# Optimization experiments

Measured on AMD Instinct MI355X. Metric: run time of the kernel, lower is better.

Reference implementation:

```python
import jax, jax.numpy as jnp
import numpy as np

N = 100000
E = 1600000
B = 64
NUM_CLASSES = 10


def setup_inputs() -> dict:
    key = jax.random.key(0)
    ks = jax.random.split(key, 8)
    x = jax.random.normal(ks[0], (N, 5), dtype=jnp.float32)
    edge_index = jax.random.randint(ks[1], (2, E), 0, N, dtype=jnp.int64)
    batch = jnp.sort(jax.random.randint(ks[2], (N,), 0, B, dtype=jnp.int64))

    def glorot(k, fan_in, fan_out):
        s = jnp.sqrt(6.0 / (fan_in + fan_out)).astype(jnp.float32)
        return jax.random.uniform(k, (fan_in, fan_out), jnp.float32, -s, s)

    dims = [(5, 32), (32, 64), (64, 128), (128, 256)]
    Ws = [glorot(jax.random.fold_in(ks[3], i), a, b) for i, (a, b) in enumerate(dims)]
    bs = [jnp.zeros((b,), jnp.float32) for (_, b) in dims]
    fc1_w = glorot(ks[4], 256, 100)
    fc1_b = jnp.zeros((100,), jnp.float32)
    fc2_w = glorot(ks[5], 100, NUM_CLASSES)
    fc2_b = jnp.zeros((NUM_CLASSES,), jnp.float32)
    return {
        'x': x, 'edge_index': edge_index, 'batch': batch,
        'W1': Ws[0], 'b1': bs[0], 'W2': Ws[1], 'b2': bs[1],
        'W3': Ws[2], 'b3': bs[2], 'W4': Ws[3], 'b4': bs[3],
        'fc1_w': fc1_w, 'fc1_b': fc1_b, 'fc2_w': fc2_w, 'fc2_b': fc2_b,
    }


def _gcn_conv(x, W, b, src, dst, dinv):
    h = x @ W                                   # [N, out]
    norm = (dinv[src] * dinv[dst])[:, None]      # [E, 1]
    msg = h[src] * norm                          # gather + scale
    agg = jax.ops.segment_sum(msg, dst, num_segments=N)
    agg = agg + h * (dinv * dinv)[:, None]       # self-loop contribution
    return agg + b


def reference(x, edge_index, batch, W1, b1, W2, b2, W3, b3, W4, b4,
              fc1_w, fc1_b, fc2_w, fc2_b):
    src, dst = edge_index[0], edge_index[1]
    # degree including self-loop
    deg = jax.ops.segment_sum(jnp.ones((E,), jnp.float32), dst, num_segments=N) + 1.0
    dinv = jax.lax.rsqrt(deg)

    h = jax.nn.relu(_gcn_conv(x, W1, b1, src, dst, dinv))
    # mesh_unpool with pool target 0 -> identity
    h = jax.nn.relu(_gcn_conv(h, W2, b2, src, dst, dinv))
    h = jax.nn.relu(_gcn_conv(h, W3, b3, src, dst, dinv))
    h = jax.nn.relu(_gcn_conv(h, W4, b4, src, dst, dinv))

    # global mean pool over graphs
    sums = jax.ops.segment_sum(h, batch, num_segments=B)
    cnt = jax.ops.segment_sum(jnp.ones((N,), jnp.float32), batch, num_segments=B)
    pooled = sums / jnp.maximum(cnt, 1.0)[:, None]

    h = jax.nn.relu(pooled @ fc1_w + fc1_b)
    return jax.nn.log_softmax(h @ fc2_w + fc2_b, axis=-1)
```

## Files before the change

### kernel.cpp

```cpp
#include <hip/hip_runtime.h>
#include <hip/hip_bf16.h>
#include <cmath>

#define NN 100000
#define NE 1600000
#define NBATCH 64
#define NB 391
#define NBP 512
#define BCAP 5120
#define NPAD (NB * BCAP)

typedef __attribute__((ext_vector_type(8))) _Float16 f16x8;
typedef __attribute__((ext_vector_type(4))) float f32x4;
typedef __attribute__((ext_vector_type(2))) float f32x2;

__device__ __forceinline__ void atomAdd(float* p, float v) {
  unsafeAtomicAdd(p, v);
}

__device__ __forceinline__ unsigned char f2fp8(float f) {
  int pk = __builtin_amdgcn_cvt_pk_fp8_f32(f, f, 0, false);
  return (unsigned char)(pk & 0xff);
}

template<int W32>
__device__ __forceinline__ void ldw(const unsigned char* p, unsigned* v) {
  if constexpr (W32 == 2) {
    uint2 t = *(const uint2*)p; v[0] = t.x; v[1] = t.y;
  } else if constexpr (W32 == 4) {
    uint4 t = *(const uint4*)p; v[0] = t.x; v[1] = t.y; v[2] = t.z; v[3] = t.w;
  } else {
    uint4 t0 = *(const uint4*)p; uint4 t1 = *(const uint4*)(p + 16);
    v[0] = t0.x; v[1] = t0.y; v[2] = t0.z; v[3] = t0.w;
    v[4] = t1.x; v[5] = t1.y; v[6] = t1.z; v[7] = t1.w;
  }
}

template<int W32>
__device__ __forceinline__ void accw(const unsigned* v, f32x2* acc) {
#pragma unroll
  for (int w = 0; w < W32; ++w) {
    acc[2 * w]     += __builtin_amdgcn_cvt_pk_f32_fp8(v[w], false);
    acc[2 * w + 1] += __builtin_amdgcn_cvt_pk_f32_fp8(v[w], true);
  }
}

__global__ __launch_bounds__(256) void k_bin(const int* __restrict__ src,
    const int* __restrict__ dst, int* __restrict__ bucketCnt, unsigned* __restrict__ pairs,
    const float* __restrict__ W2, const float* __restrict__ W3, const float* __restrict__ W4,
    _Float16* __restrict__ Wt2, _Float16* __restrict__ Wt3, _Float16* __restrict__ Wt4) {
  __shared__ int hist[NBP];
  __shared__ int scn[NBP];
  __shared__ int ofs[NBP];
  __shared__ int gbase[NBP];
  __shared__ unsigned buf[4096];
  __shared__ unsigned short bufb[4096];
  const int base = blockIdx.x * 4096;
  const int n = (NE - base < 4096) ? NE - base : 4096;
  for (int i = threadIdx.x; i < NBP; i += 256) hist[i] = 0;
  __syncthreads();

  int myS[16], myD[16];
  int nloc = 0;
  for (int i = threadIdx.x, j = 0; i < n; i += 256, ++j) {
    myS[j] = src[base + i];
    myD[j] = dst[base + i];
    atomicAdd(&hist[myD[j] >> 8], 1);
    nloc = j + 1;
  }
  __syncthreads();

  scn[threadIdx.x] = hist[threadIdx.x];
  scn[threadIdx.x + 256] = hist[threadIdx.x + 256];
  __syncthreads();
  for (int off = 1; off < NBP; off <<= 1) {
    const int i0 = threadIdx.x, i1 = threadIdx.x + 256;
    int t0 = (i0 >= off) ? scn[i0 - off] : 0;
    int t1 = (i1 >= off) ? scn[i1 - off] : 0;
    __syncthreads();
    scn[i0] += t0;
    scn[i1] += t1;
    __syncthreads();
  }
  ofs[threadIdx.x] = scn[threadIdx.x] - hist[threadIdx.x];
  ofs[threadIdx.x + 256] = scn[threadIdx.x + 256] - hist[threadIdx.x + 256];
  for (int b = threadIdx.x; b < NB; b += 256) {
    int c = hist[b];
    if (c) gbase[b] = b * BCAP + atomicAdd(&bucketCnt[b], c);
  }
  __syncthreads();

  for (int j = 0; j < nloc; ++j) {
    int b = myD[j] >> 8;
    int slot = atomicAdd(&ofs[b], 1);
    buf[slot] = ((unsigned)myS[j] << 8) | ((unsigned)myD[j] & 255u);
    bufb[slot] = (unsigned short)b;
  }
  __syncthreads();

  for (int i = threadIdx.x; i < n; i += 256) {
    int b = (int)bufb[i];
    int ex = scn[b] - hist[b];
    pairs[gbase[b] + (i - ex)] = buf[i];
  }

  int idx = blockIdx.x * 256 + threadIdx.x;
  if (idx < 2048) {
    int k = idx / 64, m = idx - k * 64;
    Wt2[m * 32 + k] = (_Float16)W2[idx];
  } else if (idx < 10240) {
    int j = idx - 2048;
    int k = j / 128, m = j - k * 128;
    Wt3[m * 64 + k] = (_Float16)W3[j];
  } else if (idx < 43008) {
    int j = idx - 10240;
    int k = j / 256, m = j - k * 256;
    Wt4[m * 128 + k] = (_Float16)W4[j];
  }
}

__global__ __launch_bounds__(256) void k_cntfill(const unsigned* __restrict__ pairs,
    const int* __restrict__ bucketCnt, const int* __restrict__ batch,
    const float* __restrict__ x, int* __restrict__ rowbeg, int* __restrict__ rowend,
    float* __restrict__ dinv, int* __restrict__ csrc, float* __restrict__ pcnt,
    _Float16* __restrict__ xs8) {
  __shared__ int c[256];
  __shared__ int scn[256];
  __shared__ int rowb[256];
  __shared__ int ofs[256];
  __shared__ int h[64];
  const int tid = threadIdx.x;
  c[tid] = 0; ofs[tid] = 0;
  if (tid < 64) h[tid] = 0;
  __syncthreads();
  const int b = blockIdx.x;
  const int s = b * BCAP;
  const int e = s + bucketCnt[b];
  for (int i = s + tid; i < e; i += 256) atomicAdd(&c[pairs[i] & 255u], 1);
  __syncthreads();
  const int v = c[tid];
  scn[tid] = v;
  __syncthreads();
  for (int off = 1; off < 256; off <<= 1) {
    int t = (tid >= off) ? scn[tid - off] : 0;
    __syncthreads();
    scn[tid] += t;
    __syncthreads();
  }
  rowb[tid] = s + scn[tid] - v;
  const int node = b * 256 + tid;
  rowbeg[node] = rowb[tid];
  rowend[node] = rowb[tid] + v;
  if (node < NN) {
    const float di = rsqrtf((float)v + 1.0f);
    dinv[node] = di;
    f16x8 o = {0, 0, 0, 0, 0, 0, 0, 0};
    o[0] = (_Float16)(x[(size_t)node * 5 + 0] * di);
    o[1] = (_Float16)(x[(size_t)node * 5 + 1] * di);
    o[2] = (_Float16)(x[(size_t)node * 5 + 2] * di);
    o[3] = (_Float16)(x[(size_t)node * 5 + 3] * di);
    o[4] = (_Float16)(x[(size_t)node * 5 + 4] * di);
    *(f16x8*)(xs8 + (size_t)node * 8) = o;
    atomicAdd(&h[batch[node]], 1);
  }
  __syncthreads();
  for (int i = s + tid; i < e; i += 256) {
    unsigned p = pairs[i];
    int t = (int)(p & 255u);
    int pos = rowb[t] + atomicAdd(&ofs[t], 1);
    csrc[pos] = (int)(p >> 8);
  }
  if (tid < 64 && h[tid]) atomAdd(&pcnt[tid], (float)h[tid]);
}

struct MegaArgs {
  const _Float16* xs8;
  const int* rowbeg; const int* rowend; const int* csrc;
  const float* dinv;
  const float* W1; const float* b1;
  unsigned char* F0;
  const _Float16* Wt2; const float* b2;
  unsigned char* F1;
  const _Float16* Wt3; const float* b3;
  unsigned char* F2;
  const _Float16* Wt4; const float* b4;
  const int* batch; float* pooled; const float* pcnt;
  const float* fc1w; const float* fc1b; const float* fc2w; const float* fc2b;
  float* out;
};

__global__ __launch_bounds__(256) void kw_l1(MegaArgs a) {
  __shared__ float w_s[160];
  __shared__ float b_s[32];
  const int tid = threadIdx.x;
  if (tid < 160) w_s[tid] = a.W1[tid];
  if (tid < 32) b_s[tid] = a.b1[tid];
  __syncthreads();
  const int r = blockIdx.x * 256 + tid;
  if (r >= NN) return;
  const float di = a.dinv[r];
  f16x8 av = *(const f16x8*)(a.xs8 + (size_t)r * 8);
  f16x8 cacc = {0, 0, 0, 0, 0, 0, 0, 0};
  int e = a.rowbeg[r];
  const int e1 = a.rowend[r];
  for (; e + 2 <= e1; e += 2) {
    const int s0 = a.csrc[e], s1 = a.csrc[e + 1];
    av   += *(const f16x8*)(a.xs8 + (size_t)s0 * 8);
    cacc += *(const f16x8*)(a.xs8 + (size_t)s1 * 8);
  }
  if (e < e1) av += *(const f16x8*)(a.xs8 + (size_t)a.csrc[e] * 8);
  av += cacc;
  const float f0 = (float)av[0] * di, f1 = (float)av[1] * di, f2 = (float)av[2] * di,
              f3 = (float)av[3] * di, f4 = (float)av[4] * di;
  float v[32];
#pragma unroll
  for (int j = 0; j < 32; ++j) {
    float s = b_s[j] + f0 * w_s[j] + f1 * w_s[32 + j] + f2 * w_s[64 + j]
                     + f3 * w_s[96 + j] + f4 * w_s[128 + j];
    v[j] = fmaxf(s, 0.f) * di;
  }
  unsigned u[8];
#pragma unroll
  for (int g2 = 0; g2 < 8; ++g2) {
    int uu = 0;
    uu = __builtin_amdgcn_cvt_pk_fp8_f32(v[4 * g2],     v[4 * g2 + 1], uu, false);
    uu = __builtin_amdgcn_cvt_pk_fp8_f32(v[4 * g2 + 2], v[4 * g2 + 3], uu, true);
    u[g2] = (unsigned)uu;
  }
  uint4* op = (uint4*)(a.F0 + (size_t)r * 32);
  op[0] = make_uint4(u[0], u[1], u[2], u[3]);
  op[1] = make_uint4(u[4], u[5], u[6], u[7]);
}

template<int K, int M, int MODE>
__global__ __launch_bounds__(256) void kw_fgemm(MegaArgs a,
    const unsigned char* __restrict__ in,
    const _Float16* __restrict__ Wt, const float* __restrict__ bias,
    unsigned char* __restrict__ outp) {
  constexpr int KC = 32;
  constexpr int KP = K + 8;
  constexpr int WP = KC + 8;
  constexpr int CTW = M / 64;
  constexpr int CB = K / 4;
  constexpr int W32 = CB / 4;
  __shared__ _Float16 a_s[64 * KP];
  __shared__ _Float16 w_s[M * WP];
  const int tid = threadIdx.x;
  const int wave = tid >> 6, lane = tid & 63;
  const int m16 = lane & 15, q = lane >> 4;
  const int r0 = blockIdx.x * 64;

  {
    const int row = tid >> 2;
    const int c = (tid & 3) * CB;
    const int r = r0 + row;
    f32x2 acc[2 * W32];
#pragma unroll
    for (int i = 0; i < 2 * W32; ++i) acc[i] = (f32x2){0.f, 0.f};
    float di = 0.f;
    if (r < NN) {
      di = a.dinv[r];
      unsigned v0[W32], v1[W32];
      ldw<W32>(in + (size_t)r * K + c, v0);
      accw<W32>(v0, acc);
      int e = a.rowbeg[r];
      const int e1 = a.rowend[r];
      for (; e + 2 <= e1; e += 2) {
        const int s0 = a.csrc[e], s1 = a.csrc[e + 1];
        ldw<W32>(in + (size_t)s0 * K + c, v0);
        ldw<W32>(in + (size_t)s1 * K + c, v1);
        accw<W32>(v0, acc);
        accw<W32>(v1, acc);
      }
      if (e < e1) {
        ldw<W32>(in + (size_t)a.csrc[e] * K + c, v0);
        accw<W32>(v0, acc);
      }
    }
    _Float16 h[CB];
#pragma unroll
    for (int i = 0; i < 2 * W32; ++i) {
      h[2 * i]     = (_Float16)(acc[i].x * di);
      h[2 * i + 1] = (_Float16)(acc[i].y * di);
    }
#pragma unroll
    for (int i = 0; i < CB / 8; ++i)
      *(uint4*)&a_s[row * KP + c + i * 8] = *(uint4*)&h[i * 8];
  }

  f32x4 acc[4][CTW];
#pragma unroll
  for (int rt = 0; rt < 4; ++rt)
#pragma unroll
    for (int ct = 0; ct < CTW; ++ct) acc[rt][ct] = (f32x4){0.f, 0.f, 0.f, 0.f};

  for (int kc = 0; kc < K; kc += KC) {
    __syncthreads();
    for (int idx = tid; idx < M * (KC / 8); idx += 256) {
      int m = idx / (KC / 8), cc = (idx % (KC / 8)) * 8;
      uint4 v = *(const uint4*)(Wt + (size_t)m * K + kc + cc);
      *(uint4*)&w_s[m * WP + cc] = v;
    }
    __syncthreads();
    f16x8 bfr[CTW];
#pragma unroll
    for (int ct = 0; ct < CTW; ++ct)
      bfr[ct] = *(const f16x8*)&w_s[(wave * (M / 4) + ct * 16 + m16) * WP + q * 8];
#pragma unroll
    for (int rt = 0; rt < 4; ++rt) {
      f16x8 afr = *(const f16x8*)&a_s[(rt * 16 + m16) * KP + kc + q * 8];
#pragma unroll
      for (int ct = 0; ct < CTW; ++ct)
        acc[rt][ct] = __builtin_amdgcn_mfma_f32_16x16x32_f16(afr, bfr[ct], acc[rt][ct], 0, 0, 0);
    }
  }

  if constexpr (MODE == 1) {
    const int rlast = (r0 + 63 < NN) ? r0 + 63 : NN - 1;
    const int bmin = a.batch[r0];
    const int bmax = a.batch[rlast];
    int rowb[4][4];
#pragma unroll
    for (int rt = 0; rt < 4; ++rt)
#pragma unroll
      for (int reg = 0; reg < 4; ++reg) {
        const int row = r0 + rt * 16 + q * 4 + reg;
        rowb[rt][reg] = (row < NN) ? a.batch[row] : -1;
      }
#pragma unroll
    for (int ct = 0; ct < CTW; ++ct) {
      const int col = wave * (M / 4) + ct * 16 + m16;
      const float bv = bias[col];
      for (int b = bmin; b <= bmax; ++b) {
        float s = 0.f;
#pragma unroll
        for (int rt = 0; rt < 4; ++rt)
#pragma unroll
          for (int reg = 0; reg < 4; ++reg)
            if (rowb[rt][reg] == b) s += fmaxf(acc[rt][ct][reg] + bv, 0.f);
        s += __shfl_xor(s, 16);
        s += __shfl_xor(s, 32);
        if (q == 0) atomAdd(&a.pooled[b * M + col], s);
      }
    }
  } else {
    float dsc[4][4];
#pragma unroll
    for (int rt = 0; rt < 4; ++rt)
#pragma unroll
      for (int reg = 0; reg < 4; ++reg) {
        const int row = r0 + rt * 16 + q * 4 + reg;
        dsc[rt][reg] = (row < NN) ? a.dinv[row] : 0.f;
      }
#pragma unroll
    for (int rt = 0; rt < 4; ++rt) {
#pragma unroll
      for (int ct = 0; ct < CTW; ++ct) {
        const int col = wave * (M / 4) + ct * 16 + m16;
        const float bv = bias[col];
#pragma unroll
        for (int reg = 0; reg < 4; ++reg) {
          const int row = r0 + rt * 16 + q * 4 + reg;
          if (row < NN) {
            float vv = fmaxf(acc[rt][ct][reg] + bv, 0.f) * dsc[rt][reg];
            outp[(size_t)row * M + col] = f2fp8(vv);
          }
        }
      }
    }
  }
}

__global__ __launch_bounds__(256) void kw_mlp(MegaArgs a) {
  __shared__ float p[256];
  __shared__ float h1[100];
  __shared__ float lo[10];
  const int tid = threadIdx.x;
  const int b = blockIdx.x;
  const float inv = 1.0f / fmaxf(a.pcnt[b], 1.0f);
  p[tid] = a.pooled[b * 256 + tid] * inv;
  __syncthreads();
  for (int j = tid; j < 100; j += 256) {
    float s = a.fc1b[j];
    for (int k = 0; k < 256; ++k) s += p[k] * a.fc1w[k * 100 + j];
    h1[j] = fmaxf(s, 0.f);
  }
  __syncthreads();
  if (tid < 10) {
    float s = a.fc2b[tid];
    for (int k = 0; k < 100; ++k) s += h1[k] * a.fc2w[k * 10 + tid];
    lo[tid] = s;
  }
  __syncthreads();
  if (tid == 0) {
    float m = lo[0];
    for (int j = 1; j < 10; ++j) m = fmaxf(m, lo[j]);
    float ssum = 0.f;
    for (int j = 0; j < 10; ++j) ssum += expf(lo[j] - m);
    float lse = m + logf(ssum);
    for (int j = 0; j < 10; ++j) a.out[b * 10 + j] = lo[j] - lse;
  }
}

extern "C" void kernel_launch(void* const* d_in, const int* in_sizes, int n_in,
                              void* d_out, int out_size, void* d_ws, size_t ws_size,
                              hipStream_t stream) {
  const float* x     = (const float*)d_in[0];
  const int*   ei    = (const int*)d_in[1];
  const int*   batch = (const int*)d_in[2];
  const float* W1 = (const float*)d_in[3];  const float* b1 = (const float*)d_in[4];
  const float* W2 = (const float*)d_in[5];  const float* b2 = (const float*)d_in[6];
  const float* W3 = (const float*)d_in[7];  const float* b3 = (const float*)d_in[8];
  const float* W4 = (const float*)d_in[9];  const float* b4 = (const float*)d_in[10];
  const float* fc1w = (const float*)d_in[11]; const float* fc1b = (const float*)d_in[12];
  const float* fc2w = (const float*)d_in[13]; const float* fc2b = (const float*)d_in[14];
  float* out = (float*)d_out;

  const int* src = ei;
  const int* dst = ei + NE;

  float* ws = (float*)d_ws;
  float* pooled = ws;
  float* pcnt   = pooled + 16384;
  int*   bucketCnt = (int*)(pcnt + 64);
  float* dinv   = (float*)(bucketCnt + 512);
  int*   rowbeg = (int*)(dinv + 100352);
  int*   rowend = rowbeg + 100352;
  int*   csrc   = rowend + 100352;
  unsigned* pairs = (unsigned*)(csrc + NPAD);
  _Float16* xs8 = (_Float16*)(pairs + NPAD);
  unsigned char* F0 = (unsigned char*)(xs8 + 800768);
  unsigned char* F1 = F0 + 3200000;
  unsigned char* F2 = F1 + 6400000;
  _Float16* Wt2 = (_Float16*)(F2 + 12800000);
  _Float16* Wt3 = Wt2 + 32 * 64;
  _Float16* Wt4 = Wt3 + 64 * 128;

  (void)hipMemsetAsync(pooled, 0, (16384 + 64 + 512) * sizeof(float), stream);
  k_bin<<<(NE + 4095) / 4096, 256, 0, stream>>>(src, dst, bucketCnt, pairs,
                                                W2, W3, W4, Wt2, Wt3, Wt4);
  k_cntfill<<<NB, 256, 0, stream>>>(pairs, bucketCnt, batch, x,
                                    rowbeg, rowend, dinv, csrc, pcnt, xs8);

  MegaArgs m;
  m.xs8 = xs8; m.rowbeg = rowbeg; m.rowend = rowend; m.csrc = csrc;
  m.dinv = dinv;
  m.W1 = W1; m.b1 = b1; m.F0 = F0;
  m.Wt2 = Wt2; m.b2 = b2; m.F1 = F1;
  m.Wt3 = Wt3; m.b3 = b3; m.F2 = F2;
  m.Wt4 = Wt4; m.b4 = b4;
  m.batch = batch; m.pooled = pooled; m.pcnt = pcnt;
  m.fc1w = fc1w; m.fc1b = fc1b; m.fc2w = fc2w; m.fc2b = fc2b;
  m.out = out;

  kw_l1<<<(NN + 255) / 256, 256, 0, stream>>>(m);
  kw_fgemm<32, 64, 0><<<(NN + 63) / 64, 256, 0, stream>>>(m, F0, Wt2, b2, F1);
  kw_fgemm<64, 128, 0><<<(NN + 63) / 64, 256, 0, stream>>>(m, F1, Wt3, b3, F2);
  kw_fgemm<128, 256, 1><<<(NN + 63) / 64, 256, 0, stream>>>(m, F2, Wt4, b4, nullptr);
  kw_mlp<<<NBATCH, 256, 0, stream>>>(m);
}
```

Baseline: 289.2 us.

## Restructure gather to 16-byte per-thread chunks and load GEMM weights directly

The fused aggregation+GEMM kernel now gives each thread a fixed 16-byte column slice and loops over rows in passes, using uniform uint4 loads with four-way unrolled neighbor gathers. The weight tile is no longer staged through shared memory; each wave reads its B fragments straight from global memory (L2/L1 cached), which removes the per-K-chunk syncthreads pairs. Layer 1 gather is also unrolled to four independent accumulators to expose more memory-level parallelism. The risk is that redundant global weight reads across blocks add cache traffic, and the multi-pass row loop may lower occupancy or parallelism for small K.

```diff
diff --git a/kernel.cpp b/kernel.cpp
--- a/kernel.cpp
+++ b/kernel.cpp
@@ -23,26 +23,15 @@
   return (unsigned char)(pk & 0xff);
 }
 
-template<int W32>
-__device__ __forceinline__ void ldw(const unsigned char* p, unsigned* v) {
-  if constexpr (W32 == 2) {
-    uint2 t = *(const uint2*)p; v[0] = t.x; v[1] = t.y;
-  } else if constexpr (W32 == 4) {
-    uint4 t = *(const uint4*)p; v[0] = t.x; v[1] = t.y; v[2] = t.z; v[3] = t.w;
-  } else {
-    uint4 t0 = *(const uint4*)p; uint4 t1 = *(const uint4*)(p + 16);
-    v[0] = t0.x; v[1] = t0.y; v[2] = t0.z; v[3] = t0.w;
-    v[4] = t1.x; v[5] = t1.y; v[6] = t1.z; v[7] = t1.w;
-  }
-}
-
-template<int W32>
-__device__ __forceinline__ void accw(const unsigned* v, f32x2* acc) {
-#pragma unroll
-  for (int w = 0; w < W32; ++w) {
-    acc[2 * w]     += __builtin_amdgcn_cvt_pk_f32_fp8(v[w], false);
-    acc[2 * w + 1] += __builtin_amdgcn_cvt_pk_f32_fp8(v[w], true);
-  }
+__device__ __forceinline__ void acc16(uint4 v, f32x2* acc) {
+  acc[0] += __builtin_amdgcn_cvt_pk_f32_fp8(v.x, false);
+  acc[1] += __builtin_amdgcn_cvt_pk_f32_fp8(v.x, true);
+  acc[2] += __builtin_amdgcn_cvt_pk_f32_fp8(v.y, false);
+  acc[3] += __builtin_amdgcn_cvt_pk_f32_fp8(v.y, true);
+  acc[4] += __builtin_amdgcn_cvt_pk_f32_fp8(v.z, false);
+  acc[5] += __builtin_amdgcn_cvt_pk_f32_fp8(v.z, true);
+  acc[6] += __builtin_amdgcn_cvt_pk_f32_fp8(v.w, false);
+  acc[7] += __builtin_amdgcn_cvt_pk_f32_fp8(v.w, true);
 }
 
 __global__ __launch_bounds__(256) void k_bin(const int* __restrict__ src,
@@ -200,16 +189,22 @@
   if (r >= NN) return;
   const float di = a.dinv[r];
   f16x8 av = *(const f16x8*)(a.xs8 + (size_t)r * 8);
-  f16x8 cacc = {0, 0, 0, 0, 0, 0, 0, 0};
+  f16x8 a1 = {0, 0, 0, 0, 0, 0, 0, 0};
+  f16x8 a2 = {0, 0, 0, 0, 0, 0, 0, 0};
+  f16x8 a3 = {0, 0, 0, 0, 0, 0, 0, 0};
   int e = a.rowbeg[r];
   const int e1 = a.rowend[r];
-  for (; e + 2 <= e1; e += 2) {
-    const int s0 = a.csrc[e], s1 = a.csrc[e + 1];
-    av   += *(const f16x8*)(a.xs8 + (size_t)s0 * 8);
-    cacc += *(const f16x8*)(a.xs8 + (size_t)s1 * 8);
-  }
-  if (e < e1) av += *(const f16x8*)(a.xs8 + (size_t)a.csrc[e] * 8);
-  av += cacc;
+  for (; e + 4 <= e1; e += 4) {
+    const int s0 = a.csrc[e], s1 = a.csrc[e + 1], s2 = a.csrc[e + 2], s3 = a.csrc[e + 3];
+    av += *(const f16x8*)(a.xs8 + (size_t)s0 * 8);
+    a1 += *(const f16x8*)(a.xs8 + (size_t)s1 * 8);
+    a2 += *(const f16x8*)(a.xs8 + (size_t)s2 * 8);
+    a3 += *(const f16x8*)(a.xs8 + (size_t)s3 * 8);
+  }
+  for (; e < e1; ++e) av += *(const f16x8*)(a.xs8 + (size_t)a.csrc[e] * 8);
+  a2 += a3;
+  av += a1;
+  av += a2;
   const float f0 = (float)av[0] * di, f1 = (float)av[1] * di, f2 = (float)av[2] * di,
               f3 = (float)av[3] * di, f4 = (float)av[4] * di;
   float v[32];
@@ -239,54 +234,58 @@
     unsigned char* __restrict__ outp) {
   constexpr int KC = 32;
   constexpr int KP = K + 8;
-  constexpr int WP = KC + 8;
   constexpr int CTW = M / 64;
-  constexpr int CB = K / 4;
-  constexpr int W32 = CB / 4;
+  constexpr int TPR = K / 16;
+  constexpr int RPP = 256 / TPR;
+  constexpr int NPASS = (64 + RPP - 1) / RPP;
   __shared__ _Float16 a_s[64 * KP];
-  __shared__ _Float16 w_s[M * WP];
   const int tid = threadIdx.x;
   const int wave = tid >> 6, lane = tid & 63;
   const int m16 = lane & 15, q = lane >> 4;
   const int r0 = blockIdx.x * 64;
 
   {
-    const int row = tid >> 2;
-    const int c = (tid & 3) * CB;
-    const int r = r0 + row;
-    f32x2 acc[2 * W32];
-#pragma unroll
-    for (int i = 0; i < 2 * W32; ++i) acc[i] = (f32x2){0.f, 0.f};
-    float di = 0.f;
-    if (r < NN) {
-      di = a.dinv[r];
-      unsigned v0[W32], v1[W32];
-      ldw<W32>(in + (size_t)r * K + c, v0);
-      accw<W32>(v0, acc);
-      int e = a.rowbeg[r];
-      const int e1 = a.rowend[r];
-      for (; e + 2 <= e1; e += 2) {
-        const int s0 = a.csrc[e], s1 = a.csrc[e + 1];
-        ldw<W32>(in + (size_t)s0 * K + c, v0);
-        ldw<W32>(in + (size_t)s1 * K + c, v1);
-        accw<W32>(v0, acc);
-        accw<W32>(v1, acc);
-      }
-      if (e < e1) {
-        ldw<W32>(in + (size_t)a.csrc[e] * K + c, v0);
-        accw<W32>(v0, acc);
+    const int rowg = tid / TPR;
+    const int c = (tid % TPR) * 16;
+    const unsigned char* bp = in + c;
+#pragma unroll
+    for (int pass = 0; pass < NPASS; ++pass) {
+      const int row = pass * RPP + rowg;
+      if (row < 64) {
+        const int r = r0 + row;
+        f32x2 acc8[8];
+#pragma unroll
+        for (int i = 0; i < 8; ++i) acc8[i] = (f32x2){0.f, 0.f};
+        float di = 0.f;
+        if (r < NN) {
+          di = a.dinv[r];
+          acc16(*(const uint4*)(bp + (size_t)r * K), acc8);
+          int e = a.rowbeg[r];
+          const int e1 = a.rowend[r];
+          for (; e + 4 <= e1; e += 4) {
+            const int s0 = a.csrc[e],     s1 = a.csrc[e + 1];
+            const int s2 = a.csrc[e + 2], s3 = a.csrc[e + 3];
+            const uint4 v0 = *(const uint4*)(bp + (size_t)s0 * K);
+            const uint4 v1 = *(const uint4*)(bp + (size_t)s1 * K);
+            const uint4 v2 = *(const uint4*)(bp + (size_t)s2 * K);
+            const uint4 v3 = *(const uint4*)(bp + (size_t)s3 * K);
+            acc16(v0, acc8); acc16(v1, acc8); acc16(v2, acc8); acc16(v3, acc8);
+          }
+          for (; e < e1; ++e)
+            acc16(*(const uint4*)(bp + (size_t)a.csrc[e] * K), acc8);
+        }
+        _Float16 h[16];
+#pragma unroll
+        for (int i = 0; i < 8; ++i) {
+          h[2 * i]     = (_Float16)(acc8[i].x * di);
+          h[2 * i + 1] = (_Float16)(acc8[i].y * di);
+        }
+        *(uint4*)&a_s[row * KP + c]     = *(uint4*)&h[0];
+        *(uint4*)&a_s[row * KP + c + 8] = *(uint4*)&h[8];
       }
     }
-    _Float16 h[CB];
-#pragma unroll
-    for (int i = 0; i < 2 * W32; ++i) {
-      h[2 * i]     = (_Float16)(acc[i].x * di);
-      h[2 * i + 1] = (_Float16)(acc[i].y * di);
-    }
-#pragma unroll
-    for (int i = 0; i < CB / 8; ++i)
-      *(uint4*)&a_s[row * KP + c + i * 8] = *(uint4*)&h[i * 8];
-  }
+  }
+  __syncthreads();
 
   f32x4 acc[4][CTW];
 #pragma unroll
@@ -294,18 +293,13 @@
 #pragma unroll
     for (int ct = 0; ct < CTW; ++ct) acc[rt][ct] = (f32x4){0.f, 0.f, 0.f, 0.f};
 
+  const _Float16* wp = Wt + (size_t)(wave * (M / 4)) * K + q * 8;
+#pragma unroll
   for (int kc = 0; kc < K; kc += KC) {
-    __syncthreads();
-    for (int idx = tid; idx < M * (KC / 8); idx += 256) {
-      int m = idx / (KC / 8), cc = (idx % (KC / 8)) * 8;
-      uint4 v = *(const uint4*)(Wt + (size_t)m * K + kc + cc);
-      *(uint4*)&w_s[m * WP + cc] = v;
-    }
-    __syncthreads();
     f16x8 bfr[CTW];
 #pragma unroll
     for (int ct = 0; ct < CTW; ++ct)
-      bfr[ct] = *(const f16x8*)&w_s[(wave * (M / 4) + ct * 16 + m16) * WP + q * 8];
+      bfr[ct] = *(const f16x8*)(wp + (size_t)(ct * 16 + m16) * K + kc);
 #pragma unroll
     for (int rt = 0; rt < 4; ++rt) {
       f16x8 afr = *(const f16x8*)&a_s[(rt * 16 + m16) * KP + kc + q * 8];
```

Result: faster. 280.9 us (-2.9%).
